# Kernel optimization log

Hardware: AMD Instinct MI355X
Metric: run time of the kernel (lower is better)

The kernel has to match this reference:

```python
import jax, jax.numpy as jnp
import numpy as np

D_MODEL = 1024
H = 16
DH = 64
EPS = 1e-5


def _layernorm(x, g, b):
    mu = jnp.mean(x, axis=-1, keepdims=True)
    var = jnp.var(x, axis=-1, keepdims=True)
    return (x - mu) * jax.lax.rsqrt(var + EPS) * g + b


def setup_inputs() -> dict:
    key = jax.random.key(0)
    ks = jax.random.split(key, 16)
    B, L = 4, 4096
    s = 0.02
    inp = {
        "x": jax.random.normal(ks[0], (B, L, D_MODEL), jnp.float32),
        "ln1_g": jnp.ones((D_MODEL,), jnp.float32),
        "ln1_b": jnp.zeros((D_MODEL,), jnp.float32),
        "Wq": jax.random.normal(ks[1], (D_MODEL, H * DH), jnp.float32) * s,
        "bq": jnp.zeros((H * DH,), jnp.float32),
        "Wk": jax.random.normal(ks[2], (D_MODEL, H * DH), jnp.float32) * s,
        "bk": jnp.zeros((H * DH,), jnp.float32),
        "Wv": jax.random.normal(ks[3], (D_MODEL, H * DH), jnp.float32) * s,
        "bv": jnp.zeros((H * DH,), jnp.float32),
        "Wg": jax.random.normal(ks[4], (D_MODEL, H * DH), jnp.float32) * s,
        "bg": jnp.zeros((H * DH,), jnp.float32),
        "decay_logit": jnp.zeros((H,), jnp.float32),
        "Wo": jax.random.normal(ks[5], (H * DH, D_MODEL), jnp.float32) * s,
        "bo": jnp.zeros((D_MODEL,), jnp.float32),
        "ln2_g": jnp.ones((D_MODEL,), jnp.float32),
        "ln2_b": jnp.zeros((D_MODEL,), jnp.float32),
        "W1": jax.random.normal(ks[6], (D_MODEL, 4 * D_MODEL), jnp.float32) * s,
        "b1": jnp.zeros((4 * D_MODEL,), jnp.float32),
        "W2": jax.random.normal(ks[7], (4 * D_MODEL, D_MODEL), jnp.float32) * s,
        "b2": jnp.zeros((D_MODEL,), jnp.float32),
    }
    return inp


def reference(x, ln1_g, ln1_b, Wq, bq, Wk, bk, Wv, bv, Wg, bg, decay_logit,
              Wo, bo, ln2_g, ln2_b, W1, b1, W2, b2):
    B, L, _ = x.shape
    y = _layernorm(x, ln1_g, ln1_b)
    # projections -> [L, B, H, DH] (time-major for scan)
    def proj(W, b):
        return (y @ W + b).reshape(B, L, H, DH).transpose(1, 0, 2, 3)
    q = proj(Wq, bq)
    k = proj(Wk, bk)
    v = proj(Wv, bv)
    g = jax.nn.sigmoid(y @ Wg + bg).reshape(B, L, H, DH).transpose(1, 0, 2, 3)
    decay = jax.nn.sigmoid(decay_logit)[None, :, None]  # [1,H,1]
    scale = DH ** -0.5

    def step(state, qkvg):
        q_t, k_t, v_t, g_t = qkvg
        state = decay * state + k_t * v_t          # [B,H,DH]
        out_t = g_t * q_t * state * scale
        return state, out_t

    state0 = jnp.zeros((B, H, DH), x.dtype)
    _, outs = jax.lax.scan(step, state0, (q, k, v, g))  # [L,B,H,DH]
    o = outs.transpose(1, 0, 2, 3).reshape(B, L, H * DH) @ Wo + bo
    x2 = x + o  # dropout is identity (eval / p=0)
    h = _layernorm(x2, ln2_g, ln2_b)
    ff = jax.nn.gelu(h @ W1 + b1, approximate=False) @ W2 + b2
    return x2 + ff
```

## Files before the change

### kernel.cpp

```cpp
#include <hip/hip_runtime.h>
#include <math.h>


#define D_MODEL 1024
#define LSEQ    4096
#define BATCH   4
#define NROWS   (BATCH * LSEQ)
#define HEADS   16
#define DH      64
#define CHUNK   128
#define NCH     (LSEQ / CHUNK)

typedef short  short8  __attribute__((ext_vector_type(8)));
typedef short  short4v __attribute__((ext_vector_type(4)));
typedef float  float4v __attribute__((ext_vector_type(4)));

__device__ inline short f2bf(float f) {
    unsigned u = __float_as_uint(f);
    u += 0x7fffu + ((u >> 16) & 1u);
    return (short)(u >> 16);
}
__device__ inline float bf2f(short s) {
    return __uint_as_float(((unsigned)(unsigned short)s) << 16);
}

__device__ inline void load_lds16(const short* g, short* l) {
    __builtin_amdgcn_global_load_lds(
        (const __attribute__((address_space(1))) void*)g,
        (__attribute__((address_space(3))) void*)l,
        16, 0, 0);
}

__global__ __launch_bounds__(1024) void transpose_f32_bf16(
    const float* __restrict__ in, short* __restrict__ out, int R, int C)
{
    __shared__ float tile[32][33];
    int tx = threadIdx.x, ty = threadIdx.y;
    int r = blockIdx.y * 32 + ty;
    int c = blockIdx.x * 32 + tx;
    tile[ty][tx] = in[(size_t)r * C + c];
    __syncthreads();
    out[(size_t)(blockIdx.x * 32 + ty) * R + blockIdx.y * 32 + tx] =
        f2bf(tile[tx][ty]);
}

__global__ __launch_bounds__(256) void concat_bias(
    const float* __restrict__ bq, const float* __restrict__ bk,
    const float* __restrict__ bv, const float* __restrict__ bg,
    float* __restrict__ out)
{
    int i = blockIdx.x * 256 + threadIdx.x;
    const float* src = (i < 1024) ? bq : (i < 2048) ? bk : (i < 3072) ? bv : bg;
    out[i] = src[i & 1023];
}

__global__ __launch_bounds__(256) void ln_kernel(
    const float* __restrict__ x, const float* __restrict__ g,
    const float* __restrict__ b, short* __restrict__ y)
{
    int row = blockIdx.x;
    int tid = threadIdx.x;
    const float4* xr = (const float4*)(x + (size_t)row * D_MODEL);
    float4 v = xr[tid];
    float s  = v.x + v.y + v.z + v.w;
    float ss = v.x * v.x + v.y * v.y + v.z * v.z + v.w * v.w;
    #pragma unroll
    for (int off = 32; off > 0; off >>= 1) {
        s  += __shfl_down(s, off);
        ss += __shfl_down(ss, off);
    }
    __shared__ float sbuf[8];
    int wv = tid >> 6, ln = tid & 63;
    if (ln == 0) { sbuf[wv] = s; sbuf[4 + wv] = ss; }
    __syncthreads();
    float tot  = sbuf[0] + sbuf[1] + sbuf[2] + sbuf[3];
    float tot2 = sbuf[4] + sbuf[5] + sbuf[6] + sbuf[7];
    float mu  = tot * (1.0f / D_MODEL);
    float var = tot2 * (1.0f / D_MODEL) - mu * mu;
    float rs  = rsqrtf(var + 1e-5f);
    float4 gg = ((const float4*)g)[tid];
    float4 bb = ((const float4*)b)[tid];
    short4v o;
    o.x = f2bf((v.x - mu) * rs * gg.x + bb.x);
    o.y = f2bf((v.y - mu) * rs * gg.y + bb.y);
    o.z = f2bf((v.z - mu) * rs * gg.z + bb.z);
    o.w = f2bf((v.w - mu) * rs * gg.w + bb.w);
    ((short4v*)y)[(size_t)row * 256 + tid] = o;
}

__global__ __launch_bounds__(256, 4) void gemm_bf16(
    const short* __restrict__ A, const short* __restrict__ BT,
    const float* __restrict__ bias, const float* __restrict__ res,
    float* __restrict__ outf, short* __restrict__ outb,
    int M, int N, int K, int mode)
{
    __shared__ short As[2 * 4096];
    __shared__ short Bs[2 * 4096];

    const int gx = gridDim.x, gy = gridDim.y;
    const int lin = blockIdx.x + blockIdx.y * gx;
    const int win = 8 * gy;
    const int grp = lin / win;
    const int rem = lin - grp * win;
    const int bx = grp * 8 + (rem & 7);
    const int by = rem >> 3;

    const int tid  = threadIdx.x;
    const int row0 = bx * 128;
    const int col0 = by * 128;
    const int lane = tid & 63;
    const int wave = tid >> 6;
    const int wm = (wave & 1) << 6;
    const int wn = (wave >> 1) << 6;
    const int lm = lane & 15;
    const int q  = lane >> 4;

    float4v acc[4][4];
    #pragma unroll
    for (int i = 0; i < 4; i++)
        #pragma unroll
        for (int j = 0; j < 4; j++)
            acc[i][j] = (float4v)(0.0f);

    const int s0 = wave * 64 + lane;
    const int s1 = 256 + wave * 64 + lane;
    const int r0 = s0 >> 2, q0 = (s0 & 3) ^ ((r0 >> 1) & 3);
    const int r1 = s1 >> 2, q1 = (s1 & 3) ^ ((r1 >> 1) & 3);
    const short* gA0 = A  + (size_t)(row0 + r0) * K + q0 * 8;
    const short* gA1 = A  + (size_t)(row0 + r1) * K + q1 * 8;
    const short* gB0 = BT + (size_t)(col0 + r0) * K + q0 * 8;
    const short* gB1 = BT + (size_t)(col0 + r1) * K + q1 * 8;
    short* lA0 = As + s0 * 8;
    short* lA1 = As + s1 * 8;
    short* lB0 = Bs + s0 * 8;
    short* lB1 = Bs + s1 * 8;

    const int swz = (lm >> 1) & 3;
    const int qs  = q ^ swz;

    load_lds16(gA0, lA0);
    load_lds16(gA1, lA1);
    load_lds16(gB0, lB0);
    load_lds16(gB1, lB1);

    int p = 0;
    for (int k0 = 0; k0 < K; k0 += 32) {
        __syncthreads();
        const int kn = k0 + 32;
        const int po = p ^ 1;
        if (kn < K) {
            load_lds16(gA0 + kn, lA0 + po * 4096);
            load_lds16(gA1 + kn, lA1 + po * 4096);
            load_lds16(gB0 + kn, lB0 + po * 4096);
            load_lds16(gB1 + kn, lB1 + po * 4096);
        }
        const short* Ab = As + p * 4096;
        const short* Bb = Bs + p * 4096;

        short8 af[4], bfr[4];
        #pragma unroll
        for (int i = 0; i < 4; i++)
            af[i] = *(const short8*)&Ab[((wm + i * 16 + lm) * 4 + qs) * 8];
        #pragma unroll
        for (int j = 0; j < 4; j++)
            bfr[j] = *(const short8*)&Bb[((wn + j * 16 + lm) * 4 + qs) * 8];
        #pragma unroll
        for (int i = 0; i < 4; i++)
            #pragma unroll
            for (int j = 0; j < 4; j++)
                acc[i][j] = __builtin_amdgcn_mfma_f32_16x16x32_bf16(
                    af[i], bfr[j], acc[i][j], 0, 0, 0);
        p ^= 1;
    }

    const int r4 = (lane >> 4) << 2;
    #pragma unroll
    for (int i = 0; i < 4; i++) {
        #pragma unroll
        for (int j = 0; j < 4; j++) {
            int colg = col0 + wn + j * 16 + lm;
            float bcol = bias[colg];
            #pragma unroll
            for (int r2 = 0; r2 < 4; r2++) {
                int rowg = row0 + wm + i * 16 + r4 + r2;
                size_t idx = (size_t)rowg * N + colg;
                float v = acc[i][j][r2] + bcol;
                if (mode == 0) {
                    if (colg >= 3072) v = 1.0f / (1.0f + expf(-v));
                    outb[idx] = f2bf(v);
                } else if (mode == 1) {
                    outf[idx] = v + res[idx];
                } else {
                    v = 0.5f * v * (1.0f + erff(v * 0.70710678118654752f));
                    outb[idx] = f2bf(v);
                }
            }
        }
    }
}

__global__ __launch_bounds__(256) void scan_pass1(
    const short* __restrict__ qkvg, const float* __restrict__ dlogit,
    float* __restrict__ carry)
{
    int j  = blockIdx.x >> 4;
    int c  = ((blockIdx.x & 15) << 8) + threadIdx.x;
    int b  = c >> 10;
    int col = c & 1023;
    float decay = 1.0f / (1.0f + expf(-dlogit[col >> 6]));
    size_t base = ((size_t)b * LSEQ + j * CHUNK) * 4096 + col;
    float s = 0.0f;
    for (int t = 0; t < CHUNK; ++t) {
        float kk = bf2f(qkvg[base + 1024]);
        float vv = bf2f(qkvg[base + 2048]);
        s = decay * s + kk * vv;
        base += 4096;
    }
    carry[j * 4096 + c] = s;
}

__global__ __launch_bounds__(256) void scan_combine(
    const float* __restrict__ carry, const float* __restrict__ dlogit,
    float* __restrict__ sinit)
{
    int c = blockIdx.x * 256 + threadIdx.x;
    float decay = 1.0f / (1.0f + expf(-dlogit[(c & 1023) >> 6]));
    float dp = powf(decay, (float)CHUNK);
    float s = 0.0f;
    for (int j = 0; j < NCH; ++j) {
        sinit[j * 4096 + c] = s;
        s = dp * s + carry[j * 4096 + c];
    }
}

__global__ __launch_bounds__(256) void scan_pass2(
    const short* __restrict__ qkvg, const float* __restrict__ dlogit,
    const float* __restrict__ sinit, short* __restrict__ att)
{
    int j  = blockIdx.x >> 4;
    int c  = ((blockIdx.x & 15) << 8) + threadIdx.x;
    int b  = c >> 10;
    int col = c & 1023;
    float decay = 1.0f / (1.0f + expf(-dlogit[col >> 6]));
    float s = sinit[j * 4096 + c];
    size_t base  = ((size_t)b * LSEQ + j * CHUNK) * 4096 + col;
    size_t obase = ((size_t)b * LSEQ + j * CHUNK) * 1024 + col;
    for (int t = 0; t < CHUNK; ++t) {
        float qq = bf2f(qkvg[base]);
        float kk = bf2f(qkvg[base + 1024]);
        float vv = bf2f(qkvg[base + 2048]);
        float gg = bf2f(qkvg[base + 3072]);
        s = decay * s + kk * vv;
        att[obase] = f2bf(gg * qq * s * 0.125f);
        base += 4096; obase += 1024;
    }
}

extern "C" void kernel_launch(void* const* d_in, const int* in_sizes, int n_in,
                              void* d_out, int out_size, void* d_ws, size_t ws_size,
                              hipStream_t stream)
{
    const float* x      = (const float*)d_in[0];
    const float* ln1_g  = (const float*)d_in[1];
    const float* ln1_b  = (const float*)d_in[2];
    const float* Wq     = (const float*)d_in[3];
    const float* bq     = (const float*)d_in[4];
    const float* Wk     = (const float*)d_in[5];
    const float* bk     = (const float*)d_in[6];
    const float* Wv     = (const float*)d_in[7];
    const float* bv     = (const float*)d_in[8];
    const float* Wg     = (const float*)d_in[9];
    const float* bg     = (const float*)d_in[10];
    const float* dlog   = (const float*)d_in[11];
    const float* Wo     = (const float*)d_in[12];
    const float* bo     = (const float*)d_in[13];
    const float* ln2_g  = (const float*)d_in[14];
    const float* ln2_b  = (const float*)d_in[15];
    const float* W1     = (const float*)d_in[16];
    const float* b1     = (const float*)d_in[17];
    const float* W2     = (const float*)d_in[18];
    const float* b2     = (const float*)d_in[19];
    float* out = (float*)d_out;

    char* ws = (char*)d_ws;
    size_t off = 0;
    auto alloc = [&](size_t bytes) -> void* {
        void* p = ws + off;
        off += (bytes + 255) & ~(size_t)255;
        return p;
    };
    short* WqkvgT = (short*)alloc((size_t)4096 * 1024 * 2);
    short* WoT    = (short*)alloc((size_t)1024 * 1024 * 2);
    short* W1T    = (short*)alloc((size_t)4096 * 1024 * 2);
    short* W2T    = (short*)alloc((size_t)1024 * 4096 * 2);
    float* biasq  = (float*)alloc((size_t)4096 * 4);
    float* carry  = (float*)alloc((size_t)NCH * 4096 * 4);
    float* sinit  = (float*)alloc((size_t)NCH * 4096 * 4);
    short* bufA   = (short*)alloc((size_t)NROWS * 1024 * 2);
    short* bufB   = (short*)alloc((size_t)NROWS * 4096 * 2);
    float* x2 = out;
    short* ybuf = bufA;
    short* att  = bufA;
    short* hbuf = bufA;
    short* qkvg = bufB;
    short* ff1  = bufB;
    (void)in_sizes; (void)n_in; (void)out_size;

    if (off > ws_size) return;

    dim3 tb(32, 32);
    transpose_f32_bf16<<<dim3(32, 32), tb, 0, stream>>>(Wq, WqkvgT + 0 * 1024 * 1024, 1024, 1024);
    transpose_f32_bf16<<<dim3(32, 32), tb, 0, stream>>>(Wk, WqkvgT + 1 * 1024 * 1024, 1024, 1024);
    transpose_f32_bf16<<<dim3(32, 32), tb, 0, stream>>>(Wv, WqkvgT + 2 * 1024 * 1024, 1024, 1024);
    transpose_f32_bf16<<<dim3(32, 32), tb, 0, stream>>>(Wg, WqkvgT + 3 * 1024 * 1024, 1024, 1024);
    transpose_f32_bf16<<<dim3(32, 32), tb, 0, stream>>>(Wo, WoT, 1024, 1024);
    transpose_f32_bf16<<<dim3(128, 32), tb, 0, stream>>>(W1, W1T, 1024, 4096);
    transpose_f32_bf16<<<dim3(32, 128), tb, 0, stream>>>(W2, W2T, 4096, 1024);
    concat_bias<<<16, 256, 0, stream>>>(bq, bk, bv, bg, biasq);

    ln_kernel<<<NROWS, 256, 0, stream>>>(x, ln1_g, ln1_b, ybuf);

    gemm_bf16<<<dim3(128, 32), 256, 0, stream>>>(
        ybuf, WqkvgT, biasq, nullptr, nullptr, qkvg, NROWS, 4096, 1024, 0);

    scan_pass1 <<<NCH * 16, 256, 0, stream>>>(qkvg, dlog, carry);
    scan_combine<<<16, 256, 0, stream>>>(carry, dlog, sinit);
    scan_pass2 <<<NCH * 16, 256, 0, stream>>>(qkvg, dlog, sinit, att);

    gemm_bf16<<<dim3(128, 8), 256, 0, stream>>>(
        att, WoT, bo, x, x2, nullptr, NROWS, 1024, 1024, 1);

    ln_kernel<<<NROWS, 256, 0, stream>>>(x2, ln2_g, ln2_b, hbuf);

    gemm_bf16<<<dim3(128, 32), 256, 0, stream>>>(
        hbuf, W1T, b1, nullptr, nullptr, ff1, NROWS, 4096, 1024, 2);

    gemm_bf16<<<dim3(128, 8), 256, 0, stream>>>(
        ff1, W2T, b2, x2, out, nullptr, NROWS, 1024, 4096, 1);
}
```

Baseline: 919.3 us.

## Rewrite bf16 GEMM with 256x256 tiles, 8 waves and interleaved prefetch

The GEMM kernel moves from 128x128 tiles with 4 waves and a K-step of 32 to 256x256 tiles with 8 waves and a K-step of 64. Global-to-LDS prefetch for A and B is split across phases and interleaved with MFMA quarters, using explicit barriers and s_setprio to raise MFMA priority. Block mapping changes to an XCD-aware round-robin (lin&7 scattering) and the LDS swizzle is updated. This aims at more data reuse per tile and better overlap of loads with compute, at the cost of higher register and LDS pressure and fewer workgroups.

```diff
diff --git a/kernel.cpp b/kernel.cpp
--- a/kernel.cpp
+++ b/kernel.cpp
@@ -88,103 +88,163 @@
     ((short4v*)y)[(size_t)row * 256 + tid] = o;
 }
 
-__global__ __launch_bounds__(256, 4) void gemm_bf16(
+__global__ __launch_bounds__(512, 2) void gemm_bf16(
     const short* __restrict__ A, const short* __restrict__ BT,
     const float* __restrict__ bias, const float* __restrict__ res,
     float* __restrict__ outf, short* __restrict__ outb,
     int M, int N, int K, int mode)
 {
-    __shared__ short As[2 * 4096];
-    __shared__ short Bs[2 * 4096];
-
-    const int gx = gridDim.x, gy = gridDim.y;
+    __shared__ short As[2][16384];
+    __shared__ short Bs[2][16384];
+
+    const int gx  = gridDim.x;
+    const int nwg = gx * gridDim.y;
     const int lin = blockIdx.x + blockIdx.y * gx;
-    const int win = 8 * gy;
-    const int grp = lin / win;
-    const int rem = lin - grp * win;
-    const int bx = grp * 8 + (rem & 7);
-    const int by = rem >> 3;
+    const int cpx = nwg >> 3;
+    const int wg  = (lin & 7) * cpx + (lin >> 3);
+    const int bx  = wg % gx;
+    const int by  = wg / gx;
+    const int row0 = bx * 256;
+    const int col0 = by * 256;
 
     const int tid  = threadIdx.x;
-    const int row0 = bx * 128;
-    const int col0 = by * 128;
+    const int wave = tid >> 6;
     const int lane = tid & 63;
-    const int wave = tid >> 6;
-    const int wm = (wave & 1) << 6;
-    const int wn = (wave >> 1) << 6;
-    const int lm = lane & 15;
-    const int q  = lane >> 4;
-
-    float4v acc[4][4];
+    const int wm   = wave >> 2;
+    const int wn   = wave & 3;
+    const int lm   = lane & 15;
+    const int q    = lane >> 4;
+    const int kq0  = ((q ^ (lm & 7)) << 3);
+
+    const int csw = (((tid & 7) ^ ((tid >> 3) & 7)) << 3);
+    const short* gA = A  + (size_t)(row0 + (tid >> 3)) * K + csw;
+    const short* gB = BT + (size_t)(col0 + (tid >> 3)) * K + csw;
+    short* sA = &As[0][0] + tid * 8;
+    short* sB = &Bs[0][0] + tid * 8;
+    const size_t K64 = (size_t)64 * K;
+
+    float4v acc[8][4];
     #pragma unroll
-    for (int i = 0; i < 4; i++)
+    for (int i = 0; i < 8; i++)
         #pragma unroll
         for (int j = 0; j < 4; j++)
             acc[i][j] = (float4v)(0.0f);
 
-    const int s0 = wave * 64 + lane;
-    const int s1 = 256 + wave * 64 + lane;
-    const int r0 = s0 >> 2, q0 = (s0 & 3) ^ ((r0 >> 1) & 3);
-    const int r1 = s1 >> 2, q1 = (s1 & 3) ^ ((r1 >> 1) & 3);
-    const short* gA0 = A  + (size_t)(row0 + r0) * K + q0 * 8;
-    const short* gA1 = A  + (size_t)(row0 + r1) * K + q1 * 8;
-    const short* gB0 = BT + (size_t)(col0 + r0) * K + q0 * 8;
-    const short* gB1 = BT + (size_t)(col0 + r1) * K + q1 * 8;
-    short* lA0 = As + s0 * 8;
-    short* lA1 = As + s1 * 8;
-    short* lB0 = Bs + s0 * 8;
-    short* lB1 = Bs + s1 * 8;
-
-    const int swz = (lm >> 1) & 3;
-    const int qs  = q ^ swz;
-
-    load_lds16(gA0, lA0);
-    load_lds16(gA1, lA1);
-    load_lds16(gB0, lB0);
-    load_lds16(gB1, lB1);
-
-    int p = 0;
-    for (int k0 = 0; k0 < K; k0 += 32) {
+    const int NT = K >> 6;
+
+    load_lds16(gA,            sA);
+    load_lds16(gA +     K64,  sA + 4096);
+    load_lds16(gA + 2 * K64,  sA + 8192);
+    load_lds16(gA + 3 * K64,  sA + 12288);
+    load_lds16(gB,            sB);
+    load_lds16(gB +     K64,  sB + 4096);
+    load_lds16(gB + 2 * K64,  sB + 8192);
+    load_lds16(gB + 3 * K64,  sB + 12288);
+    __syncthreads();
+
+    const short* Abase = &As[0][0] + wm * 8192;
+    const short* Bbase = &Bs[0][0] + (wn >> 1) * 8192;
+    const int aro = lm * 64;
+    const int bro = ((wn & 1) * 64 + lm) * 64;
+
+    short8 aF[4][2];
+    short8 bF[2][2][2];
+
+#define MFMA8(QR, QC)                                                        \
+    _Pragma("unroll")                                                        \
+    for (int ks = 0; ks < 2; ks++)                                           \
+        _Pragma("unroll")                                                    \
+        for (int i = 0; i < 4; i++)                                          \
+            _Pragma("unroll")                                                \
+            for (int j = 0; j < 2; j++)                                      \
+                acc[(QR) * 4 + i][(QC) * 2 + j] =                            \
+                    __builtin_amdgcn_mfma_f32_16x16x32_bf16(                 \
+                        aF[i][ks], bF[QC][j][ks],                            \
+                        acc[(QR) * 4 + i][(QC) * 2 + j], 0, 0, 0);
+
+    for (int t = 0; t < NT; ++t) {
+        const int bufo = (t & 1) << 14;
+        const short* Ab = Abase + bufo;
+        const short* Bb = Bbase + bufo;
+        const int  kb = (t + 1) << 6;
+        const bool pf = (t + 1 < NT);
+        const int  pfo = ((t + 1) & 1) << 14;
+
+        #pragma unroll
+        for (int i = 0; i < 4; i++) {
+            const int ar = aro + (i * 16) * 64;
+            aF[i][0] = *(const short8*)&Ab[ar + kq0];
+            aF[i][1] = *(const short8*)&Ab[ar + (kq0 ^ 32)];
+        }
+        #pragma unroll
+        for (int j = 0; j < 2; j++) {
+            const int br = bro + (j * 16) * 64;
+            bF[0][j][0] = *(const short8*)&Bb[br + kq0];
+            bF[0][j][1] = *(const short8*)&Bb[br + (kq0 ^ 32)];
+        }
+        if (pf) {
+            short* d = sA + pfo;
+            load_lds16(gA + kb,            d);
+            load_lds16(gA +     K64 + kb,  d + 4096);
+            load_lds16(gA + 2 * K64 + kb,  d + 8192);
+            load_lds16(gA + 3 * K64 + kb,  d + 12288);
+        }
+        __builtin_amdgcn_s_barrier();
+        __builtin_amdgcn_s_setprio(1);
+        MFMA8(0, 0)
+        __builtin_amdgcn_s_setprio(0);
+        __builtin_amdgcn_s_barrier();
+
+        #pragma unroll
+        for (int j = 0; j < 2; j++) {
+            const int br = bro + (32 + j * 16) * 64;
+            bF[1][j][0] = *(const short8*)&Bb[br + kq0];
+            bF[1][j][1] = *(const short8*)&Bb[br + (kq0 ^ 32)];
+        }
+        if (pf) {
+            short* d = sB + pfo;
+            load_lds16(gB + kb,            d);
+            load_lds16(gB +     K64 + kb,  d + 4096);
+            load_lds16(gB + 2 * K64 + kb,  d + 8192);
+            load_lds16(gB + 3 * K64 + kb,  d + 12288);
+        }
+        __builtin_amdgcn_s_barrier();
+        __builtin_amdgcn_s_setprio(1);
+        MFMA8(0, 1)
+        __builtin_amdgcn_s_setprio(0);
+        __builtin_amdgcn_s_barrier();
+
+        #pragma unroll
+        for (int i = 0; i < 4; i++) {
+            const int ar = aro + (64 + i * 16) * 64;
+            aF[i][0] = *(const short8*)&Ab[ar + kq0];
+            aF[i][1] = *(const short8*)&Ab[ar + (kq0 ^ 32)];
+        }
+        __builtin_amdgcn_s_barrier();
+        __builtin_amdgcn_s_setprio(1);
+        MFMA8(1, 0)
+        __builtin_amdgcn_s_setprio(0);
+        __builtin_amdgcn_s_barrier();
+
+        __builtin_amdgcn_s_setprio(1);
+        MFMA8(1, 1)
+        __builtin_amdgcn_s_setprio(0);
         __syncthreads();
-        const int kn = k0 + 32;
-        const int po = p ^ 1;
-        if (kn < K) {
-            load_lds16(gA0 + kn, lA0 + po * 4096);
-            load_lds16(gA1 + kn, lA1 + po * 4096);
-            load_lds16(gB0 + kn, lB0 + po * 4096);
-            load_lds16(gB1 + kn, lB1 + po * 4096);
-        }
-        const short* Ab = As + p * 4096;
-        const short* Bb = Bs + p * 4096;
-
-        short8 af[4], bfr[4];
-        #pragma unroll
-        for (int i = 0; i < 4; i++)
-            af[i] = *(const short8*)&Ab[((wm + i * 16 + lm) * 4 + qs) * 8];
-        #pragma unroll
-        for (int j = 0; j < 4; j++)
-            bfr[j] = *(const short8*)&Bb[((wn + j * 16 + lm) * 4 + qs) * 8];
-        #pragma unroll
-        for (int i = 0; i < 4; i++)
-            #pragma unroll
-            for (int j = 0; j < 4; j++)
-                acc[i][j] = __builtin_amdgcn_mfma_f32_16x16x32_bf16(
-                    af[i], bfr[j], acc[i][j], 0, 0, 0);
-        p ^= 1;
-    }
-
-    const int r4 = (lane >> 4) << 2;
+    }
+#undef MFMA8
+
+    const int r4 = q << 2;
     #pragma unroll
-    for (int i = 0; i < 4; i++) {
-        #pragma unroll
-        for (int j = 0; j < 4; j++) {
-            int colg = col0 + wn + j * 16 + lm;
-            float bcol = bias[colg];
+    for (int ai = 0; ai < 8; ai++) {
+        const int rowg = row0 + wm * 128 + (ai >> 2) * 64 + (ai & 3) * 16 + r4;
+        #pragma unroll
+        for (int bj = 0; bj < 4; bj++) {
+            const int colg = col0 + wn * 64 + (bj >> 1) * 32 + (bj & 1) * 16 + lm;
+            const float bcol = bias[colg];
             #pragma unroll
             for (int r2 = 0; r2 < 4; r2++) {
-                int rowg = row0 + wm + i * 16 + r4 + r2;
-                size_t idx = (size_t)rowg * N + colg;
-                float v = acc[i][j][r2] + bcol;
+                size_t idx = (size_t)(rowg + r2) * N + colg;
+                float v = acc[ai][bj][r2] + bcol;
                 if (mode == 0) {
                     if (colg >= 3072) v = 1.0f / (1.0f + expf(-v));
                     outb[idx] = f2bf(v);
@@ -320,21 +380,21 @@
 
     ln_kernel<<<NROWS, 256, 0, stream>>>(x, ln1_g, ln1_b, ybuf);
 
-    gemm_bf16<<<dim3(128, 32), 256, 0, stream>>>(
+    gemm_bf16<<<dim3(64, 16), 512, 0, stream>>>(
         ybuf, WqkvgT, biasq, nullptr, nullptr, qkvg, NROWS, 4096, 1024, 0);
 
     scan_pass1 <<<NCH * 16, 256, 0, stream>>>(qkvg, dlog, carry);
     scan_combine<<<16, 256, 0, stream>>>(carry, dlog, sinit);
     scan_pass2 <<<NCH * 16, 256, 0, stream>>>(qkvg, dlog, sinit, att);
 
-    gemm_bf16<<<dim3(128, 8), 256, 0, stream>>>(
+    gemm_bf16<<<dim3(64, 4), 512, 0, stream>>>(
         att, WoT, bo, x, x2, nullptr, NROWS, 1024, 1024, 1);
 
     ln_kernel<<<NROWS, 256, 0, stream>>>(x2, ln2_g, ln2_b, hbuf);
 
-    gemm_bf16<<<dim3(128, 32), 256, 0, stream>>>(
+    gemm_bf16<<<dim3(64, 16), 512, 0, stream>>>(
         hbuf, W1T, b1, nullptr, nullptr, ff1, NROWS, 4096, 1024, 2);
 
-    gemm_bf16<<<dim3(128, 8), 256, 0, stream>>>(
+    gemm_bf16<<<dim3(64, 4), 512, 0, stream>>>(
         ff1, W2T, b2, x2, out, nullptr, NROWS, 1024, 4096, 1);
 }
```

After: 1.034 ms. 1.13x slower.
